# Kernel optimization log

Measured on AMD Instinct MI355X. Metric: run time of the kernel, lower is better.

Reference implementation:

```python
import jax, jax.numpy as jnp
import numpy as np

B, L, D = 64, 256, 768
LABELS = 200
REL_OFF = 256  # to_pos[k] = k + 256


def setup_inputs() -> dict:
    key = jax.random.key(0)
    ks = jax.random.split(key, 8)
    return {
        "sequence_output": jax.random.normal(ks[0], (B, L, D), dtype=jnp.float32),
        "pos_embedding": jax.random.normal(ks[1], (2 * REL_OFF + 1, D), dtype=jnp.float32) * 0.02,
        "class_embedding": jax.random.normal(ks[2], (LABELS + 1, D), dtype=jnp.float32) * 0.02,
        "W": jax.random.normal(ks[3], (LABELS, 3 * D), dtype=jnp.float32) * 0.02,
        "b": jnp.zeros((LABELS,), dtype=jnp.float32),
        "head_indexes": jax.random.randint(ks[4], (B, L), 0, L),
        "frame": jax.random.randint(ks[5], (B,), 0, LABELS + 1),
        "pos": jax.random.randint(ks[6], (B,), 0, L),
    }


def reference(sequence_output, pos_embedding, class_embedding, W, b, head_indexes, frame, pos):
    # per-batch gather of token rows: sequence_output[i] = sequence_output[i][head_indexes[i]]
    gathered = jnp.take_along_axis(sequence_output, head_indexes[:, :, None], axis=1)  # [B,L,D]

    j = jnp.arange(sequence_output.shape[1])  # [L]
    rel = j[None, :] - pos[:, None] + REL_OFF  # [B,L] in [0, 512]
    pe = pos_embedding[rel]  # [B,L,D]

    # frame embedding only at j == pos[i], else class_embedding[0]
    fe_hit = class_embedding[frame]  # [B,D]
    is_pos = (j[None, :] == pos[:, None])[:, :, None]  # [B,L,1]
    fe = jnp.where(is_pos, fe_hit[:, None, :], class_embedding[0][None, None, :])  # [B,L,D]

    feat = jnp.concatenate([gathered, pe, fe], axis=-1)  # [B,L,3D]
    # dropout is identity at inference; classifier linear
    return jnp.einsum("blf,cf->blc", feat, W) + b
```

## Files before the change

kernel.cpp:

```cpp
#include <hip/hip_runtime.h>
#include <stdint.h>


typedef __attribute__((ext_vector_type(8))) short short8;
typedef __attribute__((ext_vector_type(4))) float f32x4;

#define AS1 __attribute__((address_space(1)))
#define AS3 __attribute__((address_space(3)))

#define TILE_STRIDE 36864
#define NWPK_BLK   234
#define NT         13
#define NPE_RB     9
#define NCE_RB     4
#define NLOG_BLK   ((NPE_RB + NCE_RB) * NT)
#define PEL_OFF_F  239616
#define CEL_OFF_F  349440
#define WS_NEED_B  1570816

__device__ __forceinline__ unsigned short f2bf(float f) {
    union { float f; unsigned int u; } v; v.f = f;
    unsigned int u = v.u;
    return (unsigned short)((u + 0x7fffu + ((u >> 16) & 1u)) >> 16);
}

__device__ __forceinline__ short8 pack8(f32x4 a, f32x4 b) {
    short8 r;
    r[0] = (short)f2bf(a.x); r[1] = (short)f2bf(a.y);
    r[2] = (short)f2bf(a.z); r[3] = (short)f2bf(a.w);
    r[4] = (short)f2bf(b.x); r[5] = (short)f2bf(b.y);
    r[6] = (short)f2bf(b.z); r[7] = (short)f2bf(b.w);
    return r;
}

__device__ __forceinline__ void dma16(const unsigned short* g, AS3 unsigned short* l) {
    __builtin_amdgcn_global_load_lds((AS1 const unsigned int*)g,
                                     (AS3 unsigned int*)l, 16, 0, 0);
}

__global__ __launch_bounds__(256) void prep_kernel(
    const float* __restrict__ pe,
    const float* __restrict__ ce,
    const float* __restrict__ W,
    const float* __restrict__ bias,
    unsigned short* __restrict__ ws)
{
    if (blockIdx.x < NWPK_BLK) {
        const int g   = blockIdx.x * 256 + threadIdx.x;
        const int n   = g & 15;
        const int kb8 = (g >> 4) % 288;
        const int t   = g / 4608;
        const int row = t * 16 + n;
        const int col = kb8 * 8;
        f32x4 a = {0.f, 0.f, 0.f, 0.f}, b = {0.f, 0.f, 0.f, 0.f};
        if (row < 200) {
            const float* p = W + (size_t)row * 2304 + col;
            a = *(const f32x4*)p;
            b = *(const f32x4*)(p + 4);
        }
        *(short8*)(ws + (size_t)g * 8) = pack8(a, b);
        return;
    }

    const int bb   = blockIdx.x - NWPK_BLK;
    const int w    = threadIdx.x >> 6;
    const int lane = threadIdx.x & 63;
    const int n16  = lane & 15;
    const int quad = lane >> 4;

    float* wsF = (float*)ws;
    int rowblk, t, nrows, koff;
    const float* A;
    float* outL;
    bool isCe;
    if (bb < NPE_RB * NT) {
        isCe = false; rowblk = bb / NT; t = bb % NT;
        nrows = 513; koff = 768;  A = pe; outL = wsF + PEL_OFF_F;
    } else {
        const int b2 = bb - NPE_RB * NT;
        isCe = true;  rowblk = b2 / NT; t = b2 % NT;
        nrows = 201; koff = 1536; A = ce; outL = wsF + CEL_OFF_F;
    }

    int arow = rowblk * 64 + w * 16 + n16;
    if (arow >= nrows) arow = nrows - 1;
    const float* abase = A + (size_t)arow * 768 + quad * 8;

    const int col  = t * 16 + n16;
    const int wrow = (col < 200) ? col : 0;
    const float* wbase = W + (size_t)wrow * 2304 + koff + quad * 8;

    f32x4 acc;
    {
        const float bv = (isCe && col < 200) ? bias[col] : 0.0f;
        acc = (f32x4){bv, bv, bv, bv};
    }

#pragma unroll 4
    for (int ks = 0; ks < 24; ++ks) {
        const float* ap = abase + ks * 32;
        const float* wp = wbase + ks * 32;
        short8 af = pack8(*(const f32x4*)ap, *(const f32x4*)(ap + 4));
        short8 bf = pack8(*(const f32x4*)wp, *(const f32x4*)(wp + 4));
        acc = __builtin_amdgcn_mfma_f32_16x16x32_bf16(af, bf, acc, 0, 0, 0);
    }

    const int rb = rowblk * 64 + w * 16 + quad * 4;
#pragma unroll
    for (int r = 0; r < 4; ++r) {
        const int row = rb + r;
        if (row < nrows)
            outL[(size_t)row * 208 + col] = acc[r];
    }
}

__global__ __launch_bounds__(512, 4) void gemm_kernel(
    const unsigned short* __restrict__ ws,
    const float* __restrict__ seq,
    const int*   __restrict__ head,
    const int*   __restrict__ frame,
    const int*   __restrict__ pos,
    float* __restrict__ out)
{
    __shared__ unsigned short lds[8192 + 7 * 2048];

    const unsigned short* Wp = ws;
    const float* wsF = (const float*)ws;
    const float* peL = wsF + PEL_OFF_F;
    const float* ceL = wsF + CEL_OFF_F;

    const int tid  = threadIdx.x;
    const int wave = tid >> 6;
    const int lane = tid & 63;
    const int n16  = lane & 15;
    const int quad = lane >> 4;

    const int mblk   = blockIdx.x >> 1;
    const int h      = blockIdx.x & 1;
    const int ntiles = h ? 6 : 7;
    const int tb     = h * 7;

    const int i       = mblk >> 2;
    const int pos_i   = pos[i];
    const int frame_i = frame[i];

    const int smf = wave & 3;
    const int skb = (wave >> 2) * 2;
    const int srow = mblk * 64 + smf * 16 + n16;
    const int hi   = head[srow];
    const float* aP = seq + ((size_t)i * 256 + hi) * 768 + skb * 32 + quad * 8;
    unsigned short* aDst0 = (unsigned short*)lds + ((smf * 4 + skb) * 64 + lane) * 8;
    unsigned short* aDst1 = aDst0 + 512;

    const int p = wave & 1;
    const int q = wave >> 1;
    const unsigned short* aRd0 = lds + (2 * p) * 2048 + lane * 8;
    const unsigned short* aRd1 = aRd0 + 2048;
    const unsigned short* bRd[2];
    bool uok[2];
#pragma unroll
    for (int u = 0; u < 2; ++u) {
        const int t = q + 4 * u;
        uok[u] = (t < ntiles);
        bRd[u] = lds + 8192 + (uok[u] ? t : 0) * 2048 + quad * 128 + n16 * 8;
    }

    f32x4 acc[2][2];
#pragma unroll
    for (int f = 0; f < 2; ++f)
#pragma unroll
        for (int u = 0; u < 2; ++u)
            acc[f][u] = (f32x4){0.f, 0.f, 0.f, 0.f};

    f32x4 a00 = *(const f32x4*)(aP);
    f32x4 a01 = *(const f32x4*)(aP + 4);
    f32x4 a10 = *(const f32x4*)(aP + 32);
    f32x4 a11 = *(const f32x4*)(aP + 36);

    for (int cc = 0; cc < 6; ++cc) {
        *(short8*)aDst0 = pack8(a00, a01);
        *(short8*)aDst1 = pack8(a10, a11);
        const int units = ntiles * 4;
        for (int un = wave; un < units; un += 8) {
            const int t = un >> 2, part = un & 3;
            dma16(Wp + (size_t)(tb + t) * TILE_STRIDE + cc * 2048 + part * 512 + lane * 8,
                  (AS3 unsigned short*)lds + 8192 + t * 2048 + part * 512 + lane * 8);
        }
        __syncthreads();
        if (cc < 5) {
            const float* ap = aP + (cc + 1) * 128;
            a00 = *(const f32x4*)(ap);
            a01 = *(const f32x4*)(ap + 4);
            a10 = *(const f32x4*)(ap + 32);
            a11 = *(const f32x4*)(ap + 36);
        }
#pragma unroll
        for (int ks = 0; ks < 4; ++ks) {
            short8 a0 = *(const short8*)(aRd0 + ks * 512);
            short8 a1 = *(const short8*)(aRd1 + ks * 512);
#pragma unroll
            for (int u = 0; u < 2; ++u) {
                if (uok[u]) {
                    short8 bf = *(const short8*)(bRd[u] + ks * 512);
                    acc[0][u] = __builtin_amdgcn_mfma_f32_16x16x32_bf16(a0, bf, acc[0][u], 0, 0, 0);
                    acc[1][u] = __builtin_amdgcn_mfma_f32_16x16x32_bf16(a1, bf, acc[1][u], 0, 0, 0);
                }
            }
        }
        __syncthreads();
    }

#pragma unroll
    for (int f = 0; f < 2; ++f) {
        const int rbase = mblk * 64 + (2 * p + f) * 16 + quad * 4;
#pragma unroll
        for (int u = 0; u < 2; ++u) {
            if (uok[u]) {
                const int col = (tb + q + 4 * u) * 16 + n16;
                if (col < 200) {
#pragma unroll
                    for (int r = 0; r < 4; ++r) {
                        const int row = rbase + r;
                        const int l   = row & 255;
                        const int rel = l - pos_i + 256;
                        const int cls = (l == pos_i) ? frame_i : 0;
                        out[(size_t)row * 200 + col] =
                            acc[f][u][r] + peL[(size_t)rel * 208 + col]
                                         + ceL[(size_t)cls * 208 + col];
                    }
                }
            }
        }
    }
}

__global__ __launch_bounds__(256) void gemm_fallback(
    const float* __restrict__ seq, const float* __restrict__ pe,
    const float* __restrict__ ce, const float* __restrict__ Wf,
    const float* __restrict__ bias, const int* __restrict__ head,
    const int* __restrict__ frame, const int* __restrict__ pos,
    float* __restrict__ out)
{
    const int tid  = threadIdx.x;
    const int wave = tid >> 6;
    const int lane = tid & 63;
    const int n16  = lane & 15;
    const int quad = lane >> 4;

    const int mrow  = blockIdx.x * 16 + n16;
    const int i     = mrow >> 8;
    const int j     = mrow & 255;
    const int pos_i = pos[i];
    const int hi    = head[mrow];
    const int rel   = j - pos_i + 256;
    const int cls   = (j == pos_i) ? frame[i] : 0;

    const float* segs[3];
    segs[0] = seq + ((size_t)i * 256 + (size_t)hi) * 768 + quad * 8;
    segs[1] = pe + (size_t)rel * 768 + quad * 8;
    segs[2] = ce + (size_t)cls * 768 + quad * 8;

    const int ntl = (wave == 0) ? 4 : 3;
    f32x4 acc[4];
#pragma unroll
    for (int u = 0; u < 4; ++u) {
        const int t = wave + 4 * u;
        const int col = t * 16 + n16;
        const float bv = (t < 13 && col < 200) ? bias[col] : 0.0f;
        acc[u] = (f32x4){bv, bv, bv, bv};
    }

    for (int s = 0; s < 3; ++s) {
        const float* ap = segs[s];
#pragma unroll 2
        for (int kk = 0; kk < 768; kk += 32) {
            short8 afr = pack8(*(const f32x4*)(ap + kk), *(const f32x4*)(ap + kk + 4));
#pragma unroll
            for (int u = 0; u < 4; ++u) {
                if (u < ntl) {
                    const int t = wave + 4 * u;
                    const int row = t * 16 + n16;
                    short8 bfr = {0, 0, 0, 0, 0, 0, 0, 0};
                    if (row < 200) {
                        const float* qp = Wf + (size_t)row * 2304 + s * 768 + kk + quad * 8;
                        bfr = pack8(*(const f32x4*)qp, *(const f32x4*)(qp + 4));
                    }
                    acc[u] = __builtin_amdgcn_mfma_f32_16x16x32_bf16(afr, bfr, acc[u], 0, 0, 0);
                }
            }
        }
    }

    const int rbase = blockIdx.x * 16 + quad * 4;
#pragma unroll
    for (int u = 0; u < 4; ++u) {
        const int t = wave + 4 * u;
        if (t < 13) {
            const int col = t * 16 + n16;
            if (col < 200) {
#pragma unroll
                for (int r = 0; r < 4; ++r)
                    out[(size_t)(rbase + r) * 200 + col] = acc[u][r];
            }
        }
    }
}

extern "C" void kernel_launch(void* const* d_in, const int* in_sizes, int n_in,
                              void* d_out, int out_size, void* d_ws, size_t ws_size,
                              hipStream_t stream) {
    const float* seq  = (const float*)d_in[0];
    const float* pe   = (const float*)d_in[1];
    const float* ce   = (const float*)d_in[2];
    const float* W    = (const float*)d_in[3];
    const float* bias = (const float*)d_in[4];
    const int* head   = (const int*)d_in[5];
    const int* frame  = (const int*)d_in[6];
    const int* pos    = (const int*)d_in[7];
    float* out = (float*)d_out;

    if (d_ws != nullptr && ws_size >= (size_t)WS_NEED_B) {
        unsigned short* ws = (unsigned short*)d_ws;
        prep_kernel<<<NWPK_BLK + NLOG_BLK, 256, 0, stream>>>(pe, ce, W, bias, ws);
        gemm_kernel<<<512, 512, 0, stream>>>(ws, seq, head, frame, pos, out);
    } else {
        gemm_fallback<<<1024, 256, 0, stream>>>(seq, pe, ce, W, bias, head,
                                                frame, pos, out);
    }
}
```

Baseline: 128.0 us.

## Pack only sequence weight slice; retile GEMM to 32 rows by all columns

The prep kernel now packs only the first 768 columns of W to bf16 instead of all 2304. It computes the pe/ce logit tables with smaller 16-row tiles whose K dimension is split across 8 waves and reduced through shared memory, which gives more blocks and shorter serial chains. The main GEMM changes from 64-row blocks split into two column halves to 32-row blocks covering all 13 column tiles, so each sequence row is gathered and converted once rather than twice. The cost is that each block reloads the full weight slice into LDS and uses more LDS per block, which may reduce occupancy.

```diff
diff --git a/kernel.cpp b/kernel.cpp
--- a/kernel.cpp
+++ b/kernel.cpp
@@ -8,15 +8,15 @@
 #define AS1 __attribute__((address_space(1)))
 #define AS3 __attribute__((address_space(3)))
 
-#define TILE_STRIDE 36864
-#define NWPK_BLK   234
+#define TILE_STRIDE 12288
 #define NT         13
-#define NPE_RB     9
-#define NCE_RB     4
-#define NLOG_BLK   ((NPE_RB + NCE_RB) * NT)
-#define PEL_OFF_F  239616
-#define CEL_OFF_F  349440
-#define WS_NEED_B  1570816
+#define NPE_RT     33
+#define NCE_RT     13
+#define NLOG_BLK   ((NPE_RT + NCE_RT) * NT)
+#define NPACK_BLK  39
+#define PEL_OFF_F  79872
+#define CEL_OFF_F  189696
+#define WS_NEED_B  931840
 
 __device__ __forceinline__ unsigned short f2bf(float f) {
     union { float f; unsigned int u; } v; v.f = f;
@@ -38,18 +38,20 @@
                                      (AS3 unsigned int*)l, 16, 0, 0);
 }
 
-__global__ __launch_bounds__(256) void prep_kernel(
+__global__ __launch_bounds__(512) void prep_kernel(
     const float* __restrict__ pe,
     const float* __restrict__ ce,
     const float* __restrict__ W,
     const float* __restrict__ bias,
     unsigned short* __restrict__ ws)
 {
-    if (blockIdx.x < NWPK_BLK) {
-        const int g   = blockIdx.x * 256 + threadIdx.x;
+    __shared__ float red[8 * 256];
+
+    if (blockIdx.x >= NLOG_BLK) {
+        const int g   = (blockIdx.x - NLOG_BLK) * 512 + threadIdx.x;
         const int n   = g & 15;
-        const int kb8 = (g >> 4) % 288;
-        const int t   = g / 4608;
+        const int kb8 = (g >> 4) % 96;
+        const int t   = g / 1536;
         const int row = t * 16 + n;
         const int col = kb8 * 8;
         f32x4 a = {0.f, 0.f, 0.f, 0.f}, b = {0.f, 0.f, 0.f, 0.f};
@@ -62,55 +64,64 @@
         return;
     }
 
-    const int bb   = blockIdx.x - NWPK_BLK;
+    const int bb   = blockIdx.x;
     const int w    = threadIdx.x >> 6;
     const int lane = threadIdx.x & 63;
     const int n16  = lane & 15;
     const int quad = lane >> 4;
 
     float* wsF = (float*)ws;
-    int rowblk, t, nrows, koff;
+    int rowtile, t, nrows, koff;
     const float* A;
     float* outL;
     bool isCe;
-    if (bb < NPE_RB * NT) {
-        isCe = false; rowblk = bb / NT; t = bb % NT;
+    if (bb < NPE_RT * NT) {
+        isCe = false; rowtile = bb / NT; t = bb % NT;
         nrows = 513; koff = 768;  A = pe; outL = wsF + PEL_OFF_F;
     } else {
-        const int b2 = bb - NPE_RB * NT;
-        isCe = true;  rowblk = b2 / NT; t = b2 % NT;
+        const int b2 = bb - NPE_RT * NT;
+        isCe = true;  rowtile = b2 / NT; t = b2 % NT;
         nrows = 201; koff = 1536; A = ce; outL = wsF + CEL_OFF_F;
     }
 
-    int arow = rowblk * 64 + w * 16 + n16;
+    int arow = rowtile * 16 + n16;
     if (arow >= nrows) arow = nrows - 1;
-    const float* abase = A + (size_t)arow * 768 + quad * 8;
+    const float* abase = A + (size_t)arow * 768 + w * 96 + quad * 8;
 
     const int col  = t * 16 + n16;
     const int wrow = (col < 200) ? col : 0;
-    const float* wbase = W + (size_t)wrow * 2304 + koff + quad * 8;
-
-    f32x4 acc;
-    {
+    const float* wbase = W + (size_t)wrow * 2304 + koff + w * 96 + quad * 8;
+
+    f32x4 av0[3], av1[3], wv0[3], wv1[3];
+#pragma unroll
+    for (int ks = 0; ks < 3; ++ks) {
+        av0[ks] = *(const f32x4*)(abase + ks * 32);
+        av1[ks] = *(const f32x4*)(abase + ks * 32 + 4);
+        wv0[ks] = *(const f32x4*)(wbase + ks * 32);
+        wv1[ks] = *(const f32x4*)(wbase + ks * 32 + 4);
+    }
+    f32x4 acc = (f32x4){0.f, 0.f, 0.f, 0.f};
+#pragma unroll
+    for (int ks = 0; ks < 3; ++ks)
+        acc = __builtin_amdgcn_mfma_f32_16x16x32_bf16(
+            pack8(av0[ks], av1[ks]), pack8(wv0[ks], wv1[ks]), acc, 0, 0, 0);
+
+#pragma unroll
+    for (int r = 0; r < 4; ++r)
+        red[w * 256 + lane * 4 + r] = acc[r];
+    __syncthreads();
+    if (threadIdx.x < 64) {
         const float bv = (isCe && col < 200) ? bias[col] : 0.0f;
-        acc = (f32x4){bv, bv, bv, bv};
-    }
-
-#pragma unroll 4
-    for (int ks = 0; ks < 24; ++ks) {
-        const float* ap = abase + ks * 32;
-        const float* wp = wbase + ks * 32;
-        short8 af = pack8(*(const f32x4*)ap, *(const f32x4*)(ap + 4));
-        short8 bf = pack8(*(const f32x4*)wp, *(const f32x4*)(wp + 4));
-        acc = __builtin_amdgcn_mfma_f32_16x16x32_bf16(af, bf, acc, 0, 0, 0);
-    }
-
-    const int rb = rowblk * 64 + w * 16 + quad * 4;
-#pragma unroll
-    for (int r = 0; r < 4; ++r) {
-        const int row = rb + r;
-        if (row < nrows)
-            outL[(size_t)row * 208 + col] = acc[r];
+#pragma unroll
+        for (int r = 0; r < 4; ++r) {
+            float s = 0.f;
+#pragma unroll
+            for (int ww = 0; ww < 8; ++ww)
+                s += red[ww * 256 + lane * 4 + r];
+            const int row = rowtile * 16 + quad * 4 + r;
+            if (row < nrows)
+                outL[(size_t)row * 208 + col] = s + bv;
+        }
     }
 }
 
@@ -122,7 +133,7 @@
     const int*   __restrict__ pos,
     float* __restrict__ out)
 {
-    __shared__ unsigned short lds[8192 + 7 * 2048];
+    __shared__ unsigned short lds[4096 + 13 * 2048];
 
     const unsigned short* Wp = ws;
     const float* wsF = (const float*)ws;
@@ -135,99 +146,81 @@
     const int n16  = lane & 15;
     const int quad = lane >> 4;
 
-    const int mblk   = blockIdx.x >> 1;
-    const int h      = blockIdx.x & 1;
-    const int ntiles = h ? 6 : 7;
-    const int tb     = h * 7;
-
-    const int i       = mblk >> 2;
+    const int mblk    = blockIdx.x;
+    const int i       = mblk >> 3;
     const int pos_i   = pos[i];
     const int frame_i = frame[i];
 
-    const int smf = wave & 3;
-    const int skb = (wave >> 2) * 2;
-    const int srow = mblk * 64 + smf * 16 + n16;
+    const int sfm = wave & 1;
+    const int sk  = wave >> 1;
+    const int srow = mblk * 32 + sfm * 16 + n16;
     const int hi   = head[srow];
-    const float* aP = seq + ((size_t)i * 256 + hi) * 768 + skb * 32 + quad * 8;
-    unsigned short* aDst0 = (unsigned short*)lds + ((smf * 4 + skb) * 64 + lane) * 8;
-    unsigned short* aDst1 = aDst0 + 512;
+    const float* aP = seq + ((size_t)i * 256 + hi) * 768 + sk * 32 + quad * 8;
+    unsigned short* aDst = (unsigned short*)lds + ((sfm * 4 + sk) * 64 + lane) * 8;
 
     const int p = wave & 1;
     const int q = wave >> 1;
-    const unsigned short* aRd0 = lds + (2 * p) * 2048 + lane * 8;
-    const unsigned short* aRd1 = aRd0 + 2048;
-    const unsigned short* bRd[2];
-    bool uok[2];
-#pragma unroll
-    for (int u = 0; u < 2; ++u) {
+    const unsigned short* aRd = lds + p * 2048 + lane * 8;
+    const unsigned short* bRd[4];
+    bool uok[4];
+#pragma unroll
+    for (int u = 0; u < 4; ++u) {
         const int t = q + 4 * u;
-        uok[u] = (t < ntiles);
-        bRd[u] = lds + 8192 + (uok[u] ? t : 0) * 2048 + quad * 128 + n16 * 8;
-    }
-
-    f32x4 acc[2][2];
-#pragma unroll
-    for (int f = 0; f < 2; ++f)
-#pragma unroll
-        for (int u = 0; u < 2; ++u)
-            acc[f][u] = (f32x4){0.f, 0.f, 0.f, 0.f};
-
-    f32x4 a00 = *(const f32x4*)(aP);
-    f32x4 a01 = *(const f32x4*)(aP + 4);
-    f32x4 a10 = *(const f32x4*)(aP + 32);
-    f32x4 a11 = *(const f32x4*)(aP + 36);
+        uok[u] = (t < NT);
+        bRd[u] = lds + 4096 + (uok[u] ? t : 0) * 2048 + quad * 128 + n16 * 8;
+    }
+
+    f32x4 acc[4];
+#pragma unroll
+    for (int u = 0; u < 4; ++u)
+        acc[u] = (f32x4){0.f, 0.f, 0.f, 0.f};
+
+    f32x4 a0 = *(const f32x4*)(aP);
+    f32x4 a1 = *(const f32x4*)(aP + 4);
 
     for (int cc = 0; cc < 6; ++cc) {
-        *(short8*)aDst0 = pack8(a00, a01);
-        *(short8*)aDst1 = pack8(a10, a11);
-        const int units = ntiles * 4;
-        for (int un = wave; un < units; un += 8) {
+        *(short8*)aDst = pack8(a0, a1);
+#pragma unroll
+        for (int un = wave; un < 52; un += 8) {
             const int t = un >> 2, part = un & 3;
-            dma16(Wp + (size_t)(tb + t) * TILE_STRIDE + cc * 2048 + part * 512 + lane * 8,
-                  (AS3 unsigned short*)lds + 8192 + t * 2048 + part * 512 + lane * 8);
+            dma16(Wp + (size_t)t * TILE_STRIDE + cc * 2048 + part * 512 + lane * 8,
+                  (AS3 unsigned short*)lds + 4096 + t * 2048 + part * 512 + lane * 8);
         }
         __syncthreads();
         if (cc < 5) {
             const float* ap = aP + (cc + 1) * 128;
-            a00 = *(const f32x4*)(ap);
-            a01 = *(const f32x4*)(ap + 4);
-            a10 = *(const f32x4*)(ap + 32);
-            a11 = *(const f32x4*)(ap + 36);
+            a0 = *(const f32x4*)(ap);
+            a1 = *(const f32x4*)(ap + 4);
         }
 #pragma unroll
         for (int ks = 0; ks < 4; ++ks) {
-            short8 a0 = *(const short8*)(aRd0 + ks * 512);
-            short8 a1 = *(const short8*)(aRd1 + ks * 512);
-#pragma unroll
-            for (int u = 0; u < 2; ++u) {
+            short8 af = *(const short8*)(aRd + ks * 512);
+#pragma unroll
+            for (int u = 0; u < 4; ++u) {
                 if (uok[u]) {
                     short8 bf = *(const short8*)(bRd[u] + ks * 512);
-                    acc[0][u] = __builtin_amdgcn_mfma_f32_16x16x32_bf16(a0, bf, acc[0][u], 0, 0, 0);
-                    acc[1][u] = __builtin_amdgcn_mfma_f32_16x16x32_bf16(a1, bf, acc[1][u], 0, 0, 0);
+                    acc[u] = __builtin_amdgcn_mfma_f32_16x16x32_bf16(af, bf, acc[u], 0, 0, 0);
                 }
             }
         }
         __syncthreads();
     }
 
-#pragma unroll
-    for (int f = 0; f < 2; ++f) {
-        const int rbase = mblk * 64 + (2 * p + f) * 16 + quad * 4;
-#pragma unroll
-        for (int u = 0; u < 2; ++u) {
-            if (uok[u]) {
-                const int col = (tb + q + 4 * u) * 16 + n16;
-                if (col < 200) {
-#pragma unroll
-                    for (int r = 0; r < 4; ++r) {
-                        const int row = rbase + r;
-                        const int l   = row & 255;
-                        const int rel = l - pos_i + 256;
-                        const int cls = (l == pos_i) ? frame_i : 0;
-                        out[(size_t)row * 200 + col] =
-                            acc[f][u][r] + peL[(size_t)rel * 208 + col]
-                                         + ceL[(size_t)cls * 208 + col];
-                    }
+    const int rbase = mblk * 32 + p * 16 + quad * 4;
+#pragma unroll
+    for (int u = 0; u < 4; ++u) {
+        if (uok[u]) {
+            const int col = (q + 4 * u) * 16 + n16;
+            if (col < 200) {
+#pragma unroll
+                for (int r = 0; r < 4; ++r) {
+                    const int row = rbase + r;
+                    const int l   = row & 255;
+                    const int rel = l - pos_i + 256;
+                    const int cls = (l == pos_i) ? frame_i : 0;
+                    out[(size_t)row * 200 + col] =
+                        acc[u][r] + peL[(size_t)rel * 208 + col]
+                                  + ceL[(size_t)cls * 208 + col];
                 }
             }
         }
@@ -321,7 +314,7 @@
 
     if (d_ws != nullptr && ws_size >= (size_t)WS_NEED_B) {
         unsigned short* ws = (unsigned short*)d_ws;
-        prep_kernel<<<NWPK_BLK + NLOG_BLK, 256, 0, stream>>>(pe, ce, W, bias, ws);
+        prep_kernel<<<NLOG_BLK + NPACK_BLK, 512, 0, stream>>>(pe, ce, W, bias, ws);
         gemm_kernel<<<512, 512, 0, stream>>>(ws, seq, head, frame, pos, out);
     } else {
         gemm_fallback<<<1024, 256, 0, stream>>>(seq, pe, ce, W, bias, head,
```

Measured after the change: 120.0 us. 6.2% less time.
